# Kernel tuning notes

Measured on AMD Instinct MI355X. Metric: run time of the kernel, lower is better.

## Reference

```python
import jax, jax.numpy as jnp
import numpy as np

C = 8      # num_channels
H = 512    # dim_hidden
B, S = 32, 1024
EPS = 1e-5


def _layernorm(x, gamma, beta):
    mu = jnp.mean(x, axis=-1, keepdims=True)
    var = jnp.var(x, axis=-1, keepdims=True)
    return (x - mu) * jax.lax.rsqrt(var + EPS) * gamma + beta


def setup_inputs() -> dict:
    key = jax.random.key(0)
    ks = jax.random.split(key, 7)
    x = jax.random.normal(ks[0], (C, B, S, 1), dtype=jnp.float32)
    # per-channel Linear(1,H): torch weight [H,1] -> stacked as [C,H]
    enc_w = jax.random.normal(ks[1], (C, H), dtype=jnp.float32) / jnp.sqrt(1.0)
    enc_b = jax.random.normal(ks[2], (C, H), dtype=jnp.float32) * 0.02
    enc_gamma = jnp.ones((C, H), dtype=jnp.float32)
    enc_beta = jnp.zeros((C, H), dtype=jnp.float32)
    # modulator Linear(C*H -> H): torch weight [H, C*H]
    mod_w = jax.random.normal(ks[3], (H, C * H), dtype=jnp.float32) / jnp.sqrt(C * H)
    mod_b = jax.random.normal(ks[4], (H,), dtype=jnp.float32) * 0.02
    mod_gamma = jnp.ones((H,), dtype=jnp.float32)
    mod_beta = jnp.zeros((H,), dtype=jnp.float32)
    return {
        "x": x,
        "enc_w": enc_w, "enc_b": enc_b,
        "enc_gamma": enc_gamma, "enc_beta": enc_beta,
        "mod_w": mod_w, "mod_b": mod_b,
        "mod_gamma": mod_gamma, "mod_beta": mod_beta,
    }


def reference(x, enc_w, enc_b, enc_gamma, enc_beta, mod_w, mod_b, mod_gamma, mod_beta):
    # per-channel Linear(1,H): h[c,b,s,:] = x[c,b,s,0]*enc_w[c] + enc_b[c]
    h = x * enc_w[:, None, None, :] + enc_b[:, None, None, :]      # [C,B,S,H]
    h = _layernorm(h, enc_gamma[:, None, None, :], enc_beta[:, None, None, :])
    h = jax.nn.gelu(h, approximate=False)
    # concat along last dim in channel order -> [B,S,C*H]
    h = jnp.transpose(h, (1, 2, 0, 3)).reshape(B, S, C * H)
    # channel modulator: Linear + LayerNorm + GELU
    y = jnp.einsum("bsk,hk->bsh", h, mod_w) + mod_b                # [B,S,H]
    y = _layernorm(y, mod_gamma, mod_beta)
    return jax.nn.gelu(y, approximate=False)
```

## Files before the change

### kernel.cpp

```cpp
#include <hip/hip_runtime.h>
#include <hip/hip_bf16.h>
#include <math.h>

#define C_CH 8
#define H_DIM 512
#define BS 32768
#define K_DIM 4096
#define EPS 1e-5f

#define TM 64
#define TK 32
#define NKT (K_DIM / TK)

typedef __bf16 bf16x8 __attribute__((ext_vector_type(8)));
typedef __bf16 bf16x4 __attribute__((ext_vector_type(4)));
typedef float  floatx4 __attribute__((ext_vector_type(4)));

__device__ __forceinline__ float gelu_fast(float v) {
    float x2 = v * fmaf(v * v, 0.102943215f, 2.30220815f);
    float e = __builtin_amdgcn_exp2f(-x2);
    return v * __builtin_amdgcn_rcpf(1.0f + e);
}

__global__ __launch_bounds__(256) void conv_w_kernel(const float* __restrict__ w,
                                                     __bf16* __restrict__ o) {
    int gtid  = blockIdx.x * 256 + threadIdx.x;
    int lane  = gtid & 63;
    int chunk = gtid >> 6;
    int kt    = chunk >> 5;
    int ntile = chunk & 31;
    int col   = ntile * 16 + (lane & 15);
    int k     = kt * 32 + (lane >> 4) * 8;
    const float* src = w + (size_t)col * K_DIM + k;
    float4 a = *(const float4*)src;
    float4 b = *(const float4*)(src + 4);
    bf16x8 h;
    h[0] = (__bf16)a.x; h[1] = (__bf16)a.y; h[2] = (__bf16)a.z; h[3] = (__bf16)a.w;
    h[4] = (__bf16)b.x; h[5] = (__bf16)b.y; h[6] = (__bf16)b.z; h[7] = (__bf16)b.w;
    *(bf16x8*)(o + (size_t)gtid * 8) = h;
}

template <int USE_WS>
__global__ __launch_bounds__(512, 4) void fused_gemm_kernel(
    const float* __restrict__ x,
    const float* __restrict__ enc_w,
    const float* __restrict__ enc_b,
    const float* __restrict__ enc_gamma,
    const float* __restrict__ enc_beta,
    const float* __restrict__ mod_w,
    const __bf16* __restrict__ Wb,
    const float* __restrict__ mod_b,
    const float* __restrict__ mod_gamma,
    const float* __restrict__ mod_beta,
    float* __restrict__ out)
{
    __shared__ float stats[C_CH][5];
    __shared__ float pS[C_CH][TM];
    __shared__ float qS[C_CH][TM];
    __shared__ float rS[C_CH][TM];
    __shared__ __align__(16) __bf16 Als[2 * 4 * TM * TK];
    __shared__ float redS[TM][8];
    __shared__ float redQ[TM][8];
    __shared__ float muS[TM];
    __shared__ float invS[TM];

    const int tid  = threadIdx.x;
    const int wave = tid >> 6;
    const int lane = tid & 63;

    {
        const int c = wave;
        float sw = 0.f, sb = 0.f, sww = 0.f, sbb = 0.f, swb = 0.f;
        for (int j = lane; j < H_DIM; j += 64) {
            float w = enc_w[c * H_DIM + j];
            float b = enc_b[c * H_DIM + j];
            sw += w; sb += b;
            sww = fmaf(w, w, sww);
            sbb = fmaf(b, b, sbb);
            swb = fmaf(w, b, swb);
        }
        #pragma unroll
        for (int off = 32; off; off >>= 1) {
            sw  += __shfl_xor(sw,  off);
            sb  += __shfl_xor(sb,  off);
            sww += __shfl_xor(sww, off);
            sbb += __shfl_xor(sbb, off);
            swb += __shfl_xor(swb, off);
        }
        if (lane == 0) {
            const float inv = 1.0f / (float)H_DIM;
            float mw = sw * inv, mb = sb * inv;
            stats[c][0] = mw;
            stats[c][1] = mb;
            stats[c][2] = sww * inv - mw * mw;
            stats[c][3] = sbb * inv - mb * mb;
            stats[c][4] = swb * inv - mw * mb;
        }
    }
    __syncthreads();

    const int row0 = blockIdx.x * TM;
    {
        int c = wave;
        int m = lane;
        float xv = x[c * BS + row0 + m];
        float mw = stats[c][0], mb = stats[c][1];
        float vw = stats[c][2], vb = stats[c][3], cwb = stats[c][4];
        float var = fmaf(xv, fmaf(xv, vw, 2.0f * cwb), vb);
        float q = rsqrtf(var + EPS);
        float p = xv * q;
        pS[c][m] = p;
        qS[c][m] = q;
        rS[c][m] = -fmaf(p, mw, q * mb);
    }
    __syncthreads();

    const int wn = wave;
    const int lr = lane & 15;
    const int lq = lane >> 4;

    const int arow  = tid >> 3;
    const int akq   = (tid >> 1) & 3;
    const int ahalf = tid & 1;
    const int wchunk = arow * 4 + (akq ^ ((arow >> 1) & 3));

    floatx4 acc[4][4];
    #pragma unroll
    for (int i = 0; i < 4; ++i)
        #pragma unroll
        for (int j = 0; j < 4; ++j)
            acc[i][j] = (floatx4){0.f, 0.f, 0.f, 0.f};

    auto stageA = [&](int ktn, __bf16* dst) {
        const int k0 = ktn * TK;
        const int c  = k0 >> 9;
        const int j0 = c * H_DIM + (k0 & (H_DIM - 1)) + akq * 8 + ahalf * 4;
        float p = pS[c][arow], q = qS[c][arow], r = rS[c][arow];
        float4 w = *(const float4*)(enc_w + j0);
        float4 b = *(const float4*)(enc_b + j0);
        float4 g = *(const float4*)(enc_gamma + j0);
        float4 e = *(const float4*)(enc_beta + j0);
        float fw[4] = {w.x, w.y, w.z, w.w};
        float fb[4] = {b.x, b.y, b.z, b.w};
        float fg[4] = {g.x, g.y, g.z, g.w};
        float fe[4] = {e.x, e.y, e.z, e.w};
        bf16x4 hv;
        #pragma unroll
        for (int i = 0; i < 4; ++i) {
            float t = fmaf(p, fw[i], fmaf(q, fb[i], r));
            float v = fmaf(t, fg[i], fe[i]);
            hv[i] = (__bf16)gelu_fast(v);
        }
        *(bf16x4*)(dst + wchunk * 8 + ahalf * 4) = hv;
    };

    auto loadB = [&](int ktn, int half, bf16x8* dst) {
        if (USE_WS) {
            const __bf16* base = Wb + ((size_t)(ktn * 32 + wn * 4 + half * 2) * 64 + lane) * 8;
            dst[0] = *(const bf16x8*)(base);
            dst[1] = *(const bf16x8*)(base + 512);
        } else {
            const int kk = ktn * 32 + lq * 8;
            #pragma unroll
            for (int nt = 0; nt < 2; ++nt) {
                int col = wn * 64 + (half * 2 + nt) * 16 + lr;
                const float* src = mod_w + (size_t)col * K_DIM + kk;
                float4 a = *(const float4*)src;
                float4 b = *(const float4*)(src + 4);
                bf16x8 h;
                h[0] = (__bf16)a.x; h[1] = (__bf16)a.y; h[2] = (__bf16)a.z; h[3] = (__bf16)a.w;
                h[4] = (__bf16)b.x; h[5] = (__bf16)b.y; h[6] = (__bf16)b.z; h[7] = (__bf16)b.w;
                dst[nt] = h;
            }
        }
    };

    bf16x8 bfrP[2], bfrQ[2];
    loadB(0, 0, bfrP);
    #pragma unroll
    for (int sub = 0; sub < 4; ++sub)
        stageA(sub, Als + sub * (TM * TK));
    __syncthreads();

    for (int g = 0; g < NKT / 4; ++g) {
        const __bf16* cur = Als + (g & 1) * (4 * TM * TK);
        __bf16*       nxt = Als + ((g + 1) & 1) * (4 * TM * TK);

        #pragma unroll
        for (int sub = 0; sub < 4; ++sub) {
            const int kt = g * 4 + sub;

            loadB(kt, 1, bfrQ);

            if (g + 1 < NKT / 4) stageA(kt + 4, nxt + sub * (TM * TK));

            const __bf16* Acur = cur + sub * (TM * TK);
            bf16x8 af[4];
            #pragma unroll
            for (int mt = 0; mt < 4; ++mt) {
                int row = mt * 16 + lr;
                int chunk = row * 4 + (lq ^ ((row >> 1) & 3));
                af[mt] = *(const bf16x8*)(Acur + chunk * 8);
            }

            #pragma unroll
            for (int mt = 0; mt < 4; ++mt)
                #pragma unroll
                for (int nt = 0; nt < 2; ++nt)
                    acc[mt][nt] = __builtin_amdgcn_mfma_f32_16x16x32_bf16(
                        af[mt], bfrP[nt], acc[mt][nt], 0, 0, 0);

            if (kt + 1 < NKT) loadB(kt + 1, 0, bfrP);

            #pragma unroll
            for (int mt = 0; mt < 4; ++mt)
                #pragma unroll
                for (int nt = 0; nt < 2; ++nt)
                    acc[mt][nt + 2] = __builtin_amdgcn_mfma_f32_16x16x32_bf16(
                        af[mt], bfrQ[nt], acc[mt][nt + 2], 0, 0, 0);
        }
        __syncthreads();
    }

    float mbv[4], gv[4], bev[4];
    #pragma unroll
    for (int nt = 0; nt < 4; ++nt) {
        int col = wn * 64 + nt * 16 + lr;
        mbv[nt] = mod_b[col];
        gv[nt]  = mod_gamma[col];
        bev[nt] = mod_beta[col];
    }
    #pragma unroll
    for (int mt = 0; mt < 4; ++mt)
        #pragma unroll
        for (int nt = 0; nt < 4; ++nt)
            #pragma unroll
            for (int r = 0; r < 4; ++r)
                acc[mt][nt][r] += mbv[nt];

    #pragma unroll
    for (int mt = 0; mt < 4; ++mt) {
        #pragma unroll
        for (int r = 0; r < 4; ++r) {
            float s = 0.f, ss = 0.f;
            #pragma unroll
            for (int nt = 0; nt < 4; ++nt) {
                float y = acc[mt][nt][r];
                s += y;
                ss = fmaf(y, y, ss);
            }
            #pragma unroll
            for (int off = 1; off < 16; off <<= 1) {
                s  += __shfl_xor(s,  off);
                ss += __shfl_xor(ss, off);
            }
            if (lr == 0) {
                int row = mt * 16 + lq * 4 + r;
                redS[row][wn] = s;
                redQ[row][wn] = ss;
            }
        }
    }
    __syncthreads();
    if (tid < TM) {
        float s = 0.f, ss = 0.f;
        #pragma unroll
        for (int w = 0; w < 8; ++w) {
            s  += redS[tid][w];
            ss += redQ[tid][w];
        }
        const float inv_n = 1.0f / (float)H_DIM;
        float mu  = s * inv_n;
        float var = ss * inv_n - mu * mu;
        muS[tid]  = mu;
        invS[tid] = rsqrtf(var + EPS);
    }
    __syncthreads();

    #pragma unroll
    for (int mt = 0; mt < 4; ++mt) {
        #pragma unroll
        for (int r = 0; r < 4; ++r) {
            int row = mt * 16 + lq * 4 + r;
            float mu  = muS[row];
            float inv = invS[row];
            float* op = out + (size_t)(row0 + row) * H_DIM;
            #pragma unroll
            for (int nt = 0; nt < 4; ++nt) {
                int col = wn * 64 + nt * 16 + lr;
                float t = fmaf((acc[mt][nt][r] - mu) * inv, gv[nt], bev[nt]);
                op[col] = gelu_fast(t);
            }
        }
    }
}

extern "C" void kernel_launch(void* const* d_in, const int* in_sizes, int n_in,
                              void* d_out, int out_size, void* d_ws, size_t ws_size,
                              hipStream_t stream) {
    const float* x         = (const float*)d_in[0];
    const float* enc_w     = (const float*)d_in[1];
    const float* enc_b     = (const float*)d_in[2];
    const float* enc_gamma = (const float*)d_in[3];
    const float* enc_beta  = (const float*)d_in[4];
    const float* mod_w     = (const float*)d_in[5];
    const float* mod_b     = (const float*)d_in[6];
    const float* mod_gamma = (const float*)d_in[7];
    const float* mod_beta  = (const float*)d_in[8];
    float* out = (float*)d_out;

    const size_t wb_bytes = (size_t)H_DIM * K_DIM * sizeof(__bf16);
    int use_ws = (ws_size >= wb_bytes) ? 1 : 0;
    __bf16* Wb = (__bf16*)d_ws;

    if (use_ws) {
        conv_w_kernel<<<(H_DIM * K_DIM) / (256 * 8), 256, 0, stream>>>(mod_w, Wb);
        fused_gemm_kernel<1><<<BS / TM, 512, 0, stream>>>(
            x, enc_w, enc_b, enc_gamma, enc_beta, mod_w, Wb,
            mod_b, mod_gamma, mod_beta, out);
    } else {
        fused_gemm_kernel<0><<<BS / TM, 512, 0, stream>>>(
            x, enc_w, enc_b, enc_gamma, enc_beta, mod_w, Wb,
            mod_b, mod_gamma, mod_beta, out);
    }
}
```

Before: 251.2 us.

## Precompute gamma-folded centered encoder weights and stats in prep kernel

Adds a prep kernel that, alongside the bf16 weight conversion, computes per-channel LayerNorm statistics and gamma-scaled centered encoder weights and biases into the workspace. The GEMM kernel then skips its per-block stats reduction, and its A-tile staging drops one FMA, the gamma load and the per-row r term per element. p and q are hoisted per k-group, and the B pointer arithmetic is simplified. This needs a larger workspace and extra global reads of the precomputed arrays, and falls back to the legacy path if the workspace is too small.

Result: slower. 259.6 us (+3.3%).

```diff
diff --git a/kernel.cpp b/kernel.cpp
--- a/kernel.cpp
+++ b/kernel.cpp
@@ -11,6 +11,7 @@
 #define TM 64
 #define TK 32
 #define NKT (K_DIM / TK)
+#define TMTK (TM * TK)
 
 typedef __bf16 bf16x8 __attribute__((ext_vector_type(8)));
 typedef __bf16 bf16x4 __attribute__((ext_vector_type(4)));
@@ -22,22 +23,73 @@
     return v * __builtin_amdgcn_rcpf(1.0f + e);
 }
 
-__global__ __launch_bounds__(256) void conv_w_kernel(const float* __restrict__ w,
-                                                     __bf16* __restrict__ o) {
-    int gtid  = blockIdx.x * 256 + threadIdx.x;
-    int lane  = gtid & 63;
-    int chunk = gtid >> 6;
-    int kt    = chunk >> 5;
-    int ntile = chunk & 31;
-    int col   = ntile * 16 + (lane & 15);
-    int k     = kt * 32 + (lane >> 4) * 8;
-    const float* src = w + (size_t)col * K_DIM + k;
-    float4 a = *(const float4*)src;
-    float4 b = *(const float4*)(src + 4);
-    bf16x8 h;
-    h[0] = (__bf16)a.x; h[1] = (__bf16)a.y; h[2] = (__bf16)a.z; h[3] = (__bf16)a.w;
-    h[4] = (__bf16)b.x; h[5] = (__bf16)b.y; h[6] = (__bf16)b.z; h[7] = (__bf16)b.w;
-    *(bf16x8*)(o + (size_t)gtid * 8) = h;
+__global__ __launch_bounds__(256) void prep_kernel(
+    const float* __restrict__ w, __bf16* __restrict__ o,
+    const float* __restrict__ enc_w, const float* __restrict__ enc_b,
+    const float* __restrict__ enc_gamma,
+    float* __restrict__ Wf, float* __restrict__ Bf, float* __restrict__ st)
+{
+    __shared__ float red[4][5];
+    if (blockIdx.x < 1024) {
+        int gtid  = blockIdx.x * 256 + threadIdx.x;
+        int lane  = gtid & 63;
+        int chunk = gtid >> 6;
+        int kt    = chunk >> 5;
+        int ntile = chunk & 31;
+        int col   = ntile * 16 + (lane & 15);
+        int k     = kt * 32 + (lane >> 4) * 8;
+        const float* src = w + (size_t)col * K_DIM + k;
+        float4 a = *(const float4*)src;
+        float4 b = *(const float4*)(src + 4);
+        bf16x8 h;
+        h[0] = (__bf16)a.x; h[1] = (__bf16)a.y; h[2] = (__bf16)a.z; h[3] = (__bf16)a.w;
+        h[4] = (__bf16)b.x; h[5] = (__bf16)b.y; h[6] = (__bf16)b.z; h[7] = (__bf16)b.w;
+        *(bf16x8*)(o + (size_t)gtid * 8) = h;
+    } else {
+        const int c = blockIdx.x - 1024;
+        const int t = threadIdx.x;
+        const float* wp = enc_w + c * H_DIM;
+        const float* bp = enc_b + c * H_DIM;
+        const float* gp = enc_gamma + c * H_DIM;
+        float w0 = wp[t], w1 = wp[t + 256];
+        float b0 = bp[t], b1 = bp[t + 256];
+        float sw  = w0 + w1;
+        float sb  = b0 + b1;
+        float sww = fmaf(w0, w0, w1 * w1);
+        float sbb = fmaf(b0, b0, b1 * b1);
+        float swb = fmaf(w0, b0, w1 * b1);
+        #pragma unroll
+        for (int off = 32; off; off >>= 1) {
+            sw  += __shfl_xor(sw,  off);
+            sb  += __shfl_xor(sb,  off);
+            sww += __shfl_xor(sww, off);
+            sbb += __shfl_xor(sbb, off);
+            swb += __shfl_xor(swb, off);
+        }
+        int wv = t >> 6, ln = t & 63;
+        if (ln == 0) {
+            red[wv][0] = sw;  red[wv][1] = sb;  red[wv][2] = sww;
+            red[wv][3] = sbb; red[wv][4] = swb;
+        }
+        __syncthreads();
+        float tsw  = red[0][0] + red[1][0] + red[2][0] + red[3][0];
+        float tsb  = red[0][1] + red[1][1] + red[2][1] + red[3][1];
+        float tsww = red[0][2] + red[1][2] + red[2][2] + red[3][2];
+        float tsbb = red[0][3] + red[1][3] + red[2][3] + red[3][3];
+        float tswb = red[0][4] + red[1][4] + red[2][4] + red[3][4];
+        const float inv = 1.0f / (float)H_DIM;
+        float mw = tsw * inv, mb = tsb * inv;
+        if (t == 0) {
+            st[c * 4 + 0] = tsww * inv - mw * mw;
+            st[c * 4 + 1] = 2.0f * (tswb * inv - mw * mb);
+            st[c * 4 + 2] = tsbb * inv - mb * mb;
+        }
+        float g0 = gp[t], g1 = gp[t + 256];
+        Wf[c * H_DIM + t]       = g0 * (w0 - mw);
+        Wf[c * H_DIM + t + 256] = g1 * (w1 - mw);
+        Bf[c * H_DIM + t]       = g0 * (b0 - mb);
+        Bf[c * H_DIM + t + 256] = g1 * (b1 - mb);
+    }
 }
 
 template <int USE_WS>
@@ -49,6 +101,9 @@
     const float* __restrict__ enc_beta,
     const float* __restrict__ mod_w,
     const __bf16* __restrict__ Wb,
+    const float* __restrict__ Wf,
+    const float* __restrict__ Bf,
+    const float* __restrict__ st,
     const float* __restrict__ mod_b,
     const float* __restrict__ mod_gamma,
     const float* __restrict__ mod_beta,
@@ -58,7 +113,7 @@
     __shared__ float pS[C_CH][TM];
     __shared__ float qS[C_CH][TM];
     __shared__ float rS[C_CH][TM];
-    __shared__ __align__(16) __bf16 Als[2 * 4 * TM * TK];
+    __shared__ __align__(16) __bf16 Als[2 * 4 * TMTK];
     __shared__ float redS[TM][8];
     __shared__ float redQ[TM][8];
     __shared__ float muS[TM];
@@ -67,51 +122,60 @@
     const int tid  = threadIdx.x;
     const int wave = tid >> 6;
     const int lane = tid & 63;
-
-    {
-        const int c = wave;
-        float sw = 0.f, sb = 0.f, sww = 0.f, sbb = 0.f, swb = 0.f;
-        for (int j = lane; j < H_DIM; j += 64) {
-            float w = enc_w[c * H_DIM + j];
-            float b = enc_b[c * H_DIM + j];
-            sw += w; sb += b;
-            sww = fmaf(w, w, sww);
-            sbb = fmaf(b, b, sbb);
-            swb = fmaf(w, b, swb);
-        }
-        #pragma unroll
-        for (int off = 32; off; off >>= 1) {
-            sw  += __shfl_xor(sw,  off);
-            sb  += __shfl_xor(sb,  off);
-            sww += __shfl_xor(sww, off);
-            sbb += __shfl_xor(sbb, off);
-            swb += __shfl_xor(swb, off);
-        }
-        if (lane == 0) {
-            const float inv = 1.0f / (float)H_DIM;
-            float mw = sw * inv, mb = sb * inv;
-            stats[c][0] = mw;
-            stats[c][1] = mb;
-            stats[c][2] = sww * inv - mw * mw;
-            stats[c][3] = sbb * inv - mb * mb;
-            stats[c][4] = swb * inv - mw * mb;
-        }
-    }
-    __syncthreads();
-
     const int row0 = blockIdx.x * TM;
-    {
+
+    if (USE_WS) {
         int c = wave;
         int m = lane;
         float xv = x[c * BS + row0 + m];
-        float mw = stats[c][0], mb = stats[c][1];
-        float vw = stats[c][2], vb = stats[c][3], cwb = stats[c][4];
-        float var = fmaf(xv, fmaf(xv, vw, 2.0f * cwb), vb);
-        float q = rsqrtf(var + EPS);
-        float p = xv * q;
-        pS[c][m] = p;
+        float vw = st[c * 4 + 0], cwb2 = st[c * 4 + 1], vb = st[c * 4 + 2];
+        float q = rsqrtf(fmaf(xv, fmaf(xv, vw, cwb2), vb) + EPS);
+        pS[c][m] = xv * q;
         qS[c][m] = q;
-        rS[c][m] = -fmaf(p, mw, q * mb);
+    } else {
+        {
+            const int c = wave;
+            float sw = 0.f, sb = 0.f, sww = 0.f, sbb = 0.f, swb = 0.f;
+            for (int j = lane; j < H_DIM; j += 64) {
+                float w = enc_w[c * H_DIM + j];
+                float b = enc_b[c * H_DIM + j];
+                sw += w; sb += b;
+                sww = fmaf(w, w, sww);
+                sbb = fmaf(b, b, sbb);
+                swb = fmaf(w, b, swb);
+            }
+            #pragma unroll
+            for (int off = 32; off; off >>= 1) {
+                sw  += __shfl_xor(sw,  off);
+                sb  += __shfl_xor(sb,  off);
+                sww += __shfl_xor(sww, off);
+                sbb += __shfl_xor(sbb, off);
+                swb += __shfl_xor(swb, off);
+            }
+            if (lane == 0) {
+                const float inv = 1.0f / (float)H_DIM;
+                float mw = sw * inv, mb = sb * inv;
+                stats[c][0] = mw;
+                stats[c][1] = mb;
+                stats[c][2] = sww * inv - mw * mw;
+                stats[c][3] = sbb * inv - mb * mb;
+                stats[c][4] = swb * inv - mw * mb;
+            }
+        }
+        __syncthreads();
+        {
+            int c = wave;
+            int m = lane;
+            float xv = x[c * BS + row0 + m];
+            float mw = stats[c][0], mb = stats[c][1];
+            float vw = stats[c][2], vb = stats[c][3], cwb = stats[c][4];
+            float var = fmaf(xv, fmaf(xv, vw, 2.0f * cwb), vb);
+            float q = rsqrtf(var + EPS);
+            float p = xv * q;
+            pS[c][m] = p;
+            qS[c][m] = q;
+            rS[c][m] = -fmaf(p, mw, q * mb);
+        }
     }
     __syncthreads();
 
@@ -131,7 +195,24 @@
         for (int j = 0; j < 4; ++j)
             acc[i][j] = (floatx4){0.f, 0.f, 0.f, 0.f};
 
-    auto stageA = [&](int ktn, __bf16* dst) {
+    auto stageA2 = [&](int ktn, __bf16* dst, float p, float q) {
+        const int j0 = ktn * TK + akq * 8 + ahalf * 4;
+        float4 w = *(const float4*)(Wf + j0);
+        float4 b = *(const float4*)(Bf + j0);
+        float4 e = *(const float4*)(enc_beta + j0);
+        float fw[4] = {w.x, w.y, w.z, w.w};
+        float fb[4] = {b.x, b.y, b.z, b.w};
+        float fe[4] = {e.x, e.y, e.z, e.w};
+        bf16x4 hv;
+        #pragma unroll
+        for (int i = 0; i < 4; ++i) {
+            float v = fmaf(p, fw[i], fmaf(q, fb[i], fe[i]));
+            hv[i] = (__bf16)gelu_fast(v);
+        }
+        *(bf16x4*)(dst + wchunk * 8 + ahalf * 4) = hv;
+    };
+
+    auto stageA_legacy = [&](int ktn, __bf16* dst) {
         const int k0 = ktn * TK;
         const int c  = k0 >> 9;
         const int j0 = c * H_DIM + (k0 & (H_DIM - 1)) + akq * 8 + ahalf * 4;
@@ -154,11 +235,12 @@
         *(bf16x4*)(dst + wchunk * 8 + ahalf * 4) = hv;
     };
 
+    const __bf16* baseB = Wb + ((size_t)(wn * 4) * 64 + lane) * 8;
     auto loadB = [&](int ktn, int half, bf16x8* dst) {
         if (USE_WS) {
-            const __bf16* base = Wb + ((size_t)(ktn * 32 + wn * 4 + half * 2) * 64 + lane) * 8;
-            dst[0] = *(const bf16x8*)(base);
-            dst[1] = *(const bf16x8*)(base + 512);
+            const __bf16* bp = baseB + ktn * 16384 + half * 1024;
+            dst[0] = *(const bf16x8*)(bp);
+            dst[1] = *(const bf16x8*)(bp + 512);
         } else {
             const int kk = ktn * 32 + lq * 8;
             #pragma unroll
@@ -177,14 +259,29 @@
 
     bf16x8 bfrP[2], bfrQ[2];
     loadB(0, 0, bfrP);
-    #pragma unroll
-    for (int sub = 0; sub < 4; ++sub)
-        stageA(sub, Als + sub * (TM * TK));
+    if (USE_WS) {
+        float p0 = pS[0][arow], q0 = qS[0][arow];
+        #pragma unroll
+        for (int sub = 0; sub < 4; ++sub)
+            stageA2(sub, Als + sub * TMTK, p0, q0);
+    } else {
+        #pragma unroll
+        for (int sub = 0; sub < 4; ++sub)
+            stageA_legacy(sub, Als + sub * TMTK);
+    }
     __syncthreads();
 
     for (int g = 0; g < NKT / 4; ++g) {
-        const __bf16* cur = Als + (g & 1) * (4 * TM * TK);
-        __bf16*       nxt = Als + ((g + 1) & 1) * (4 * TM * TK);
+        const __bf16* cur = Als + (g & 1) * (4 * TMTK);
+        __bf16*       nxt = Als + ((g + 1) & 1) * (4 * TMTK);
+        const bool haveNext = (g + 1 < NKT / 4);
+
+        float pC = 0.f, qC = 0.f;
+        if (USE_WS && haveNext) {
+            const int cn = (g + 1) >> 2;
+            pC = pS[cn][arow];
+            qC = qS[cn][arow];
+        }
 
         #pragma unroll
         for (int sub = 0; sub < 4; ++sub) {
@@ -192,9 +289,12 @@
 
             loadB(kt, 1, bfrQ);
 
-            if (g + 1 < NKT / 4) stageA(kt + 4, nxt + sub * (TM * TK));
-
-            const __bf16* Acur = cur + sub * (TM * TK);
+            if (haveNext) {
+                if (USE_WS) stageA2(kt + 4, nxt + sub * TMTK, pC, qC);
+                else        stageA_legacy(kt + 4, nxt + sub * TMTK);
+            }
+
+            const __bf16* Acur = cur + sub * TMTK;
             bf16x8 af[4];
             #pragma unroll
             for (int mt = 0; mt < 4; ++mt) {
@@ -310,17 +410,27 @@
     float* out = (float*)d_out;
 
     const size_t wb_bytes = (size_t)H_DIM * K_DIM * sizeof(__bf16);
-    int use_ws = (ws_size >= wb_bytes) ? 1 : 0;
+    const size_t wf_off   = wb_bytes;
+    const size_t bf_off   = wf_off + (size_t)C_CH * H_DIM * sizeof(float);
+    const size_t st_off   = bf_off + (size_t)C_CH * H_DIM * sizeof(float);
+    const size_t need     = st_off + (size_t)C_CH * 4 * sizeof(float);
+
+    int use_ws = (ws_size >= need) ? 1 : 0;
     __bf16* Wb = (__bf16*)d_ws;
+    float*  Wf = (float*)((char*)d_ws + wf_off);
+    float*  Bf = (float*)((char*)d_ws + bf_off);
+    float*  st = (float*)((char*)d_ws + st_off);
 
     if (use_ws) {
-        conv_w_kernel<<<(H_DIM * K_DIM) / (256 * 8), 256, 0, stream>>>(mod_w, Wb);
+        prep_kernel<<<1024 + C_CH, 256, 0, stream>>>(
+            mod_w, Wb, enc_w, enc_b, enc_gamma, Wf, Bf, st);
         fused_gemm_kernel<1><<<BS / TM, 512, 0, stream>>>(
-            x, enc_w, enc_b, enc_gamma, enc_beta, mod_w, Wb,
+            x, enc_w, enc_b, enc_gamma, enc_beta, mod_w, Wb, Wf, Bf, st,
             mod_b, mod_gamma, mod_beta, out);
     } else {
         fused_gemm_kernel<0><<<BS / TM, 512, 0, stream>>>(
             x, enc_w, enc_b, enc_gamma, enc_beta, mod_w, Wb,
+            (const float*)0, (const float*)0, (const float*)0,
             mod_b, mod_gamma, mod_beta, out);
     }
 }
```
